# Performance work log

Hardware: AMD Instinct MI355X
Metric: run time of the kernel (lower is better)

## Reference

```python
import jax, jax.numpy as jnp
import numpy as np

# GridEncoder(d=3, L=16, F=2, b=2, N_min=16, log2_hashmap_size=19, gridtype='hash'), bound=1
D = 3
L = 16
F = 2
N_MIN = 16
PLS = 2.0            # per_level_scale b
LOG2_T = 19
BOUND = 1.0
N_CORNERS = 2 ** D
# fast_hash primes from the CUDA kernel (first D entries)
PRIMES = (np.uint32(1), np.uint32(2654435761), np.uint32(805459861))


def _offsets_and_res():
    """Replicates the Python offsets loop and the kernel's per-level resolution."""
    S = np.log2(PLS)
    offs = [0]
    res = []
    off = 0
    for l in range(L):
        scale = np.exp2(l * S) * N_MIN - 1.0      # kernel: scale = exp2f(level*S)*H - 1
        res.append(int(np.ceil(scale)) + 1)       # kernel: resolution = ceil(scale)+1
        N_l = int(np.ceil(N_MIN * PLS ** l))
        T = min(2 ** LOG2_T, (N_l + 1) ** D)
        off += T
        offs.append(off)
    return offs, res

OFFSETS, RES = _offsets_and_res()  # OFFSETS[-1] == 7131219


def setup_inputs() -> dict:
    k1, k2 = jax.random.split(jax.random.key(0))
    inputs = jax.random.uniform(k1, (1_000_000, D), jnp.float32, -1.0, 1.0)
    embeddings = jax.random.uniform(k2, (OFFSETS[-1], F), jnp.float32, -1e-4, 1e-4)
    return {"inputs": inputs, "embeddings": embeddings}


def _encode(inputs, embeddings):
    # normalize to [0,1] as in GridEncoder.forward
    x = (inputs + BOUND) / (2 * BOUND)            # [B, D]
    B = x.shape[0]
    S = np.log2(PLS)
    outs = []
    for l in range(L):  # fixed small level count -> Python loop is fine
        hmap = OFFSETS[l + 1] - OFFSETS[l]
        emb = embeddings[OFFSETS[l]:OFFSETS[l + 1]]   # static slice [hmap, F]
        resolution = RES[l]
        scale = np.float32(np.exp2(l * S) * N_MIN - 1.0)
        pos = x * scale + 0.5
        pg = jnp.floor(pos)
        frac = pos - pg                               # [B, D] in [0,1)
        pg = pg.astype(jnp.uint32)
        use_hash = (resolution + 1) ** D > hmap       # static per level
        acc = jnp.zeros((B, F), x.dtype)
        for corner in range(N_CORNERS):               # 8 corners, multilinear interp
            w = jnp.ones((B,), x.dtype)
            idx = jnp.zeros((B,), jnp.uint32)
            stride = 1
            for d in range(D):
                bit = (corner >> d) & 1
                g = pg[:, d] + np.uint32(bit)         # corner grid coord (uint32)
                w = w * (frac[:, d] if bit else (1.0 - frac[:, d]))
                if use_hash:
                    idx = idx ^ (g * PRIMES[d])       # uint32 wraparound == fast_hash
                else:
                    idx = idx + g * np.uint32(stride)
                    stride *= (resolution + 1)
            idx = (idx % np.uint32(hmap)).astype(jnp.int32)
            acc = acc + w[:, None] * emb[idx]         # gather [B, F]
        outs.append(acc)
    return jnp.concatenate(outs, axis=-1)             # [B, L*F], level-major like permute+reshape


def reference(inputs, embeddings):
    return _encode(inputs, embeddings)
```

## Files before the change

### kernel.cpp

```cpp
#include <hip/hip_runtime.h>
#include <cstdint>


static constexpr uint32_t kOff[17] = {
    0u, 4913u, 40850u, 315475u, 839763u, 1364051u, 1888339u, 2412627u,
    2936915u, 3461203u, 3985491u, 4509779u, 5034067u, 5558355u, 6082643u,
    6606931u, 7131219u};

static constexpr uint32_t P1 = 2654435761u;
static constexpr uint32_t P2 = 805459861u;

typedef float f4a8 __attribute__((ext_vector_type(4), aligned(8)));
typedef float v2f __attribute__((ext_vector_type(2)));
typedef float v4f __attribute__((ext_vector_type(4)));

__device__ __forceinline__ float2 ntload2(const float2* p) {
  v2f t = __builtin_nontemporal_load((const v2f*)p);
  return make_float2(t[0], t[1]);
}
__device__ __forceinline__ void ntstore2(float2* p, float a, float b) {
  v2f t;
  t[0] = a;
  t[1] = b;
  __builtin_nontemporal_store(t, (v2f*)p);
}
__device__ __forceinline__ void ntstore4(float4* p, float a, float b, float c,
                                         float d) {
  v4f t;
  t[0] = a;
  t[1] = b;
  t[2] = c;
  t[3] = d;
  __builtin_nontemporal_store(t, (v4f*)p);
}

__device__ __forceinline__ float to_unit(float v) {
  return __fmul_rn(__fadd_rn(v, 1.0f), 0.5f);
}

__device__ __forceinline__ void pos_decomp_rt(float x0, float x1, float x2,
                                              float scale, uint32_t& i0,
                                              uint32_t& i1, uint32_t& i2,
                                              float& f0, float& f1, float& f2) {
  float p0 = __fadd_rn(__fmul_rn(x0, scale), 0.5f);
  float p1 = __fadd_rn(__fmul_rn(x1, scale), 0.5f);
  float p2 = __fadd_rn(__fmul_rn(x2, scale), 0.5f);
  float g0 = floorf(p0), g1 = floorf(p1), g2 = floorf(p2);
  f0 = __fsub_rn(p0, g0);
  f1 = __fsub_rn(p1, g1);
  f2 = __fsub_rn(p2, g2);
  i0 = (uint32_t)g0;
  i1 = (uint32_t)g1;
  i2 = (uint32_t)g2;
}

__device__ __forceinline__ void hashed_accum_rt(float x0, float x1, float x2,
                                                float scale,
                                                const float2* __restrict__ t2,
                                                float& A0, float& A1) {
  constexpr uint32_t mask = 0x7FFFFu;
  uint32_t i0, i1, i2;
  float f0, f1, f2;
  pos_decomp_rt(x0, x1, x2, scale, i0, i1, i2, f0, f1, f2);

  const float w0l = __fsub_rn(1.0f, f0), w0h = f0;
  const float w1v[2] = {__fsub_rn(1.0f, f1), f1};
  const float w2v[2] = {__fsub_rn(1.0f, f2), f2};
  uint32_t h1v[2], h2v[2];
  h1v[0] = i1 * P1;
  h1v[1] = h1v[0] + P1;
  h2v[0] = i2 * P2;
  h2v[1] = h2v[0] + P2;

  const bool odd = (i0 & 1u) != 0u;
  float acc0 = A0, acc1 = A1;
#pragma unroll
  for (int b2 = 0; b2 < 2; ++b2) {
#pragma unroll
    for (int b1 = 0; b1 < 2; ++b1) {
      const uint32_t ex = h1v[b1] ^ h2v[b2];
      const uint32_t ilo = (i0 ^ ex) & mask;
      const f4a8 v = *(const f4a8*)(t2 + (ilo & ~1u));
      const bool hs = (ilo & 1u) != 0u;
      float eL0 = hs ? v.z : v.x;
      float eL1 = hs ? v.w : v.y;
      float eH0 = hs ? v.x : v.z;
      float eH1 = hs ? v.y : v.w;
      if (odd) {
        const uint32_t ihi = ((i0 + 1u) ^ ex) & mask;
        const float2 e = t2[ihi];
        eH0 = e.x;
        eH1 = e.y;
      }
      const float wl = __fmul_rn(__fmul_rn(w0l, w1v[b1]), w2v[b2]);
      const float wh = __fmul_rn(__fmul_rn(w0h, w1v[b1]), w2v[b2]);
      acc0 = __fadd_rn(acc0, __fmul_rn(wl, eL0));
      acc1 = __fadd_rn(acc1, __fmul_rn(wl, eL1));
      acc0 = __fadd_rn(acc0, __fmul_rn(wh, eH0));
      acc1 = __fadd_rn(acc1, __fmul_rn(wh, eH1));
    }
  }
  A0 = acc0;
  A1 = acc1;
}

template <int LV>
__device__ __forceinline__ void dense_accum(float x0, float x1, float x2,
                                            const float* __restrict__ embf,
                                            float& A0, float& A1) {
  static_assert(LV < 3, "");
  constexpr uint32_t res = 16u << LV;
  constexpr uint32_t off = kOff[LV];
  constexpr uint32_t s1 = res + 1u, s2 = s1 * s1;
  constexpr float scale = (float)res - 1.0f;
  uint32_t i0, i1, i2;
  float f0, f1, f2;
  pos_decomp_rt(x0, x1, x2, scale, i0, i1, i2, f0, f1, f2);

  const float w0l = __fsub_rn(1.0f, f0), w0h = f0;
  const float w1v[2] = {__fsub_rn(1.0f, f1), f1};
  const float w2v[2] = {__fsub_rn(1.0f, f2), f2};
  const uint32_t base = i0 + i1 * s1 + i2 * s2;
  const float2* t2 = (const float2*)embf + off;

  float acc0 = A0, acc1 = A1;
#pragma unroll
  for (int b2 = 0; b2 < 2; ++b2) {
#pragma unroll
    for (int b1 = 0; b1 < 2; ++b1) {
      const uint32_t idx = base + (b1 ? s1 : 0u) + (b2 ? s2 : 0u);
      const f4a8 v = *(const f4a8*)(t2 + idx);
      const float wl = __fmul_rn(__fmul_rn(w0l, w1v[b1]), w2v[b2]);
      const float wh = __fmul_rn(__fmul_rn(w0h, w1v[b1]), w2v[b2]);
      acc0 = __fadd_rn(acc0, __fmul_rn(wl, v.x));
      acc1 = __fadd_rn(acc1, __fmul_rn(wl, v.y));
      acc0 = __fadd_rn(acc0, __fmul_rn(wh, v.z));
      acc1 = __fadd_rn(acc1, __fmul_rn(wh, v.w));
    }
  }
  A0 = acc0;
  A1 = acc1;
}


__global__ __launch_bounds__(256) void mega_kernel(
    const float* __restrict__ in, const float* __restrict__ embf,
    float2* __restrict__ ws, int B, int NB) {
  const int zone = blockIdx.x / NB;
  const int q = (blockIdx.x - zone * NB) * 256 + threadIdx.x;
  const int p0 = q << 1;
  if (p0 >= B) return;
  const bool hasB = (p0 + 1) < B;

  float xA0, xA1, xA2, xB0 = 0.f, xB1 = 0.f, xB2 = 0.f;
  if (hasB) {
    const float2* in2 = (const float2*)in;
    const size_t b3 = (size_t)q * 3;
    const float2 u0 = ntload2(in2 + b3);
    const float2 u1 = ntload2(in2 + b3 + 1);
    const float2 u2 = ntload2(in2 + b3 + 2);
    xA0 = to_unit(u0.x);
    xA1 = to_unit(u0.y);
    xA2 = to_unit(u1.x);
    xB0 = to_unit(u1.y);
    xB1 = to_unit(u2.x);
    xB2 = to_unit(u2.y);
  } else {
    xA0 = to_unit(in[(size_t)p0 * 3 + 0]);
    xA1 = to_unit(in[(size_t)p0 * 3 + 1]);
    xA2 = to_unit(in[(size_t)p0 * 3 + 2]);
  }
  const bool pair4 = hasB && ((B & 1) == 0);

  const int level = zone + 3;
  const float scale = (float)(int)((16u << level) - 1u);
  const float2* t2 =
      (const float2*)embf + (315475u + (uint32_t)(level - 3) * 524288u);
  float2* wsl = ws + (size_t)level * B;

  float a0 = 0.0f, a1 = 0.0f;
  hashed_accum_rt(xA0, xA1, xA2, scale, t2, a0, a1);
  if (pair4) {
    float b0 = 0.0f, b1 = 0.0f;
    hashed_accum_rt(xB0, xB1, xB2, scale, t2, b0, b1);
    ntstore4((float4*)(wsl + p0), a0, a1, b0, b1);
  } else {
    ntstore2(wsl + p0, a0, a1);
    if (hasB) {
      float b0 = 0.0f, b1 = 0.0f;
      hashed_accum_rt(xB0, xB1, xB2, scale, t2, b0, b1);
      ntstore2(wsl + p0 + 1, b0, b1);
    }
  }
}


__global__ __launch_bounds__(256) void final_kernel(
    const float* __restrict__ in, const float* __restrict__ embf,
    const float2* __restrict__ ws, float4* __restrict__ out4, int B) {
  __shared__ float4 lds[4 * 257];
  const int tid = (int)threadIdx.x;
  const int p = blockIdx.x * 256 + tid;

  float a[32];
#pragma unroll
  for (int i = 0; i < 32; ++i) a[i] = 0.0f;

  if (p < B) {
    const float x0 = to_unit(in[(size_t)p * 3 + 0]);
    const float x1 = to_unit(in[(size_t)p * 3 + 1]);
    const float x2 = to_unit(in[(size_t)p * 3 + 2]);
    dense_accum<0>(x0, x1, x2, embf, a[0], a[1]);
    dense_accum<1>(x0, x1, x2, embf, a[2], a[3]);
    dense_accum<2>(x0, x1, x2, embf, a[4], a[5]);
#pragma unroll
    for (int l = 3; l < 16; ++l) {
      const float2 e = ws[(size_t)l * B + p];
      a[2 * l] = e.x;
      a[2 * l + 1] = e.y;
    }
  }

  const size_t gbase = (size_t)blockIdx.x * 2048;
  const size_t lim = (size_t)B * 8;
#pragma unroll
  for (int half = 0; half < 2; ++half) {
    if (half) __syncthreads();
#pragma unroll
    for (int w = 0; w < 4; ++w) {
      const int qd = half * 4 + w;
      lds[w * 257 + tid] =
          make_float4(a[4 * qd], a[4 * qd + 1], a[4 * qd + 2], a[4 * qd + 3]);
    }
    __syncthreads();
#pragma unroll
    for (int k = 0; k < 4; ++k) {
      const int gl = k * 256 + tid;
      const int pt = gl >> 2;
      const int qw = gl & 3;
      const size_t g = gbase + (size_t)pt * 8 + (size_t)(half * 4 + qw);
      if (g < lim) out4[g] = lds[qw * 257 + pt];
    }
  }
}


template <int LV>
__device__ __forceinline__ void any_accum(float x0, float x1, float x2,
                                          const float* __restrict__ embf,
                                          float& A0, float& A1) {
  if constexpr (LV < 3) {
    dense_accum<LV>(x0, x1, x2, embf, A0, A1);
  } else {
    constexpr float scale = (float)(16u << LV) - 1.0f;
    const float2* t2 = (const float2*)embf + kOff[LV];
    hashed_accum_rt(x0, x1, x2, scale, t2, A0, A1);
  }
}

template <int LBASE>
__global__ __launch_bounds__(256) void grid_enc_kernel(
    const float* __restrict__ in, const float* __restrict__ embf,
    float* __restrict__ out, int B) {
  const int p = blockIdx.x * 256 + threadIdx.x;
  if (p >= B) return;
  const float x0 = to_unit(in[(size_t)p * 3 + 0]);
  const float x1 = to_unit(in[(size_t)p * 3 + 1]);
  const float x2 = to_unit(in[(size_t)p * 3 + 2]);

  float a[16];
#pragma unroll
  for (int i = 0; i < 16; ++i) a[i] = 0.0f;

  any_accum<LBASE + 0>(x0, x1, x2, embf, a[0], a[1]);
  any_accum<LBASE + 1>(x0, x1, x2, embf, a[2], a[3]);
  any_accum<LBASE + 2>(x0, x1, x2, embf, a[4], a[5]);
  any_accum<LBASE + 3>(x0, x1, x2, embf, a[6], a[7]);
  any_accum<LBASE + 4>(x0, x1, x2, embf, a[8], a[9]);
  any_accum<LBASE + 5>(x0, x1, x2, embf, a[10], a[11]);
  any_accum<LBASE + 6>(x0, x1, x2, embf, a[12], a[13]);
  any_accum<LBASE + 7>(x0, x1, x2, embf, a[14], a[15]);

  float4* __restrict__ o = (float4*)(out + (size_t)p * 32 + LBASE * 2);
  o[0] = make_float4(a[0], a[1], a[2], a[3]);
  o[1] = make_float4(a[4], a[5], a[6], a[7]);
  o[2] = make_float4(a[8], a[9], a[10], a[11]);
  o[3] = make_float4(a[12], a[13], a[14], a[15]);
}

extern "C" void kernel_launch(void* const* d_in, const int* in_sizes, int n_in,
                              void* d_out, int out_size, void* d_ws,
                              size_t ws_size, hipStream_t stream) {
  const float* in = (const float*)d_in[0];
  const float* emb = (const float*)d_in[1];
  float* out = (float*)d_out;
  const int B = in_sizes[0] / 3;
  const size_t ws_needed = (size_t)16 * (size_t)B * sizeof(float2);

  if (ws_size >= ws_needed) {
    float2* ws = (float2*)d_ws;
    const int NB = ((B + 1) / 2 + 255) / 256;
    mega_kernel<<<NB * 13, 256, 0, stream>>>(in, emb, ws, B, NB);
    const int blocksP = (B + 255) / 256;
    final_kernel<<<blocksP, 256, 0, stream>>>(in, emb, ws, (float4*)out, B);
  } else {
    const int blocksP = (B + 255) / 256;
    grid_enc_kernel<0><<<blocksP, 256, 0, stream>>>(in, emb, out, B);
    grid_enc_kernel<8><<<blocksP, 256, 0, stream>>>(in, emb, out, B);
  }
}
```

Before: 769.2 us.

## Process four points per thread in hashed levels and single-pass LDS transpose

Adds a mega4 kernel that handles four points per thread for the hashed levels. It loads the inputs as three float4s and writes the results as two float4s, used when B is a multiple of 4. This cuts the thread count, amortises index setup, and gives more independent gathers per thread for memory-level parallelism, at the cost of more registers and fewer waves. The final kernel now stages all 8 float4 quads in LDS at once with a single barrier and writes fully contiguous output, doubling LDS use per block.

```diff
diff --git a/kernel.cpp b/kernel.cpp
--- a/kernel.cpp
+++ b/kernel.cpp
@@ -17,6 +17,10 @@
 __device__ __forceinline__ float2 ntload2(const float2* p) {
   v2f t = __builtin_nontemporal_load((const v2f*)p);
   return make_float2(t[0], t[1]);
+}
+__device__ __forceinline__ float4 ntload4(const float4* p) {
+  v4f t = __builtin_nontemporal_load((const v4f*)p);
+  return make_float4(t[0], t[1], t[2], t[3]);
 }
 __device__ __forceinline__ void ntstore2(float2* p, float a, float b) {
   v2f t;
@@ -143,7 +147,41 @@
 }
 
 
-__global__ __launch_bounds__(256) void mega_kernel(
+__global__ __launch_bounds__(256) void mega4_kernel(
+    const float* __restrict__ in, const float* __restrict__ embf,
+    float2* __restrict__ ws, int B, int NB) {
+  const int zone = blockIdx.x / NB;
+  const int q = (blockIdx.x - zone * NB) * 256 + threadIdx.x;
+  const int p0 = q << 2;
+  if (p0 >= B) return;
+
+  const float4* in4 = (const float4*)in;
+  const size_t b3 = (size_t)q * 3;
+  const float4 u0 = ntload4(in4 + b3);
+  const float4 u1 = ntload4(in4 + b3 + 1);
+  const float4 u2 = ntload4(in4 + b3 + 2);
+
+  const int level = zone + 3;
+  const float scale = (float)(int)((16u << level) - 1u);
+  const float2* t2 =
+      (const float2*)embf + (315475u + (uint32_t)(level - 3) * 524288u);
+  float2* wsl = ws + (size_t)level * B;
+
+  float a0 = 0.f, a1 = 0.f, b0 = 0.f, b1 = 0.f;
+  float c0 = 0.f, c1 = 0.f, d0 = 0.f, d1 = 0.f;
+  hashed_accum_rt(to_unit(u0.x), to_unit(u0.y), to_unit(u0.z), scale, t2, a0,
+                  a1);
+  hashed_accum_rt(to_unit(u0.w), to_unit(u1.x), to_unit(u1.y), scale, t2, b0,
+                  b1);
+  hashed_accum_rt(to_unit(u1.z), to_unit(u1.w), to_unit(u2.x), scale, t2, c0,
+                  c1);
+  hashed_accum_rt(to_unit(u2.y), to_unit(u2.z), to_unit(u2.w), scale, t2, d0,
+                  d1);
+  ntstore4((float4*)(wsl + p0), a0, a1, b0, b1);
+  ntstore4((float4*)(wsl + p0 + 2), c0, c1, d0, d1);
+}
+
+__global__ __launch_bounds__(256) void mega2_kernel(
     const float* __restrict__ in, const float* __restrict__ embf,
     float2* __restrict__ ws, int B, int NB) {
   const int zone = blockIdx.x / NB;
@@ -198,7 +236,7 @@
 __global__ __launch_bounds__(256) void final_kernel(
     const float* __restrict__ in, const float* __restrict__ embf,
     const float2* __restrict__ ws, float4* __restrict__ out4, int B) {
-  __shared__ float4 lds[4 * 257];
+  __shared__ float4 lds[8 * 257];
   const int tid = (int)threadIdx.x;
   const int p = blockIdx.x * 256 + tid;
 
@@ -221,26 +259,19 @@
     }
   }
 
+#pragma unroll
+  for (int w = 0; w < 8; ++w)
+    lds[w * 257 + tid] =
+        make_float4(a[4 * w], a[4 * w + 1], a[4 * w + 2], a[4 * w + 3]);
+  __syncthreads();
+
   const size_t gbase = (size_t)blockIdx.x * 2048;
   const size_t lim = (size_t)B * 8;
 #pragma unroll
-  for (int half = 0; half < 2; ++half) {
-    if (half) __syncthreads();
-#pragma unroll
-    for (int w = 0; w < 4; ++w) {
-      const int qd = half * 4 + w;
-      lds[w * 257 + tid] =
-          make_float4(a[4 * qd], a[4 * qd + 1], a[4 * qd + 2], a[4 * qd + 3]);
-    }
-    __syncthreads();
-#pragma unroll
-    for (int k = 0; k < 4; ++k) {
-      const int gl = k * 256 + tid;
-      const int pt = gl >> 2;
-      const int qw = gl & 3;
-      const size_t g = gbase + (size_t)pt * 8 + (size_t)(half * 4 + qw);
-      if (g < lim) out4[g] = lds[qw * 257 + pt];
-    }
+  for (int j = 0; j < 8; ++j) {
+    const int gl = j * 256 + tid;
+    const size_t g = gbase + gl;
+    if (g < lim) out4[g] = lds[(gl & 7) * 257 + (gl >> 3)];
   }
 }
 
@@ -299,8 +330,13 @@
 
   if (ws_size >= ws_needed) {
     float2* ws = (float2*)d_ws;
-    const int NB = ((B + 1) / 2 + 255) / 256;
-    mega_kernel<<<NB * 13, 256, 0, stream>>>(in, emb, ws, B, NB);
+    if ((B & 3) == 0) {
+      const int NB = (B / 4 + 255) / 256;
+      mega4_kernel<<<NB * 13, 256, 0, stream>>>(in, emb, ws, B, NB);
+    } else {
+      const int NB = ((B + 1) / 2 + 255) / 256;
+      mega2_kernel<<<NB * 13, 256, 0, stream>>>(in, emb, ws, B, NB);
+    }
     const int blocksP = (B + 255) / 256;
     final_kernel<<<blocksP, 256, 0, stream>>>(in, emb, ws, (float4*)out, B);
   } else {
```

Measured after the change: 756.0 us. Within noise of the previous version (-1.7%).
